# Kernel tuning notes

Hardware: AMD Instinct MI355X
Metric: run time of the kernel (lower is better)

The kernel has to match this reference:

```python
import jax, jax.numpy as jnp
import numpy as np

B, S, D, H = 4, 2048, 1024, 16
DK = D // H  # 64


def setup_inputs() -> dict:
    key = jax.random.key(0)
    ks = jax.random.split(key, 7)
    scale = 1.0 / np.sqrt(D)
    q = jax.random.normal(ks[0], (B, S, D), dtype=jnp.float32)
    k = jax.random.normal(ks[1], (B, S, D), dtype=jnp.float32)
    v = jax.random.normal(ks[2], (B, S, D), dtype=jnp.float32)
    # causal mask, broadcastable to [B, H, S, S]
    mask = jnp.tril(jnp.ones((S, S), dtype=jnp.int32))[None, None, :, :]
    Wq = jax.random.normal(ks[3], (D, D), dtype=jnp.float32) * scale
    Wk = jax.random.normal(ks[4], (D, D), dtype=jnp.float32) * scale
    Wv = jax.random.normal(ks[5], (D, D), dtype=jnp.float32) * scale
    Wo = jax.random.normal(ks[6], (D, D), dtype=jnp.float32) * scale
    return {"q": q, "k": k, "v": v, "mask": mask,
            "Wq": Wq, "Wk": Wk, "Wv": Wv, "Wo": Wo}


def reference(q, k, v, mask, Wq, Wk, Wv, Wo):
    # nn.Linear(bias=False): y = x @ W.T
    query = jnp.einsum('bsd,ed->bse', q, Wq).reshape(B, S, H, DK).transpose(0, 2, 1, 3)
    key_ = jnp.einsum('bsd,ed->bse', k, Wk).reshape(B, S, H, DK).transpose(0, 2, 1, 3)
    value = jnp.einsum('bsd,ed->bse', v, Wv).reshape(B, S, H, DK).transpose(0, 2, 1, 3)
    scores = jnp.einsum('bhqd,bhkd->bhqk', query, key_) / jnp.sqrt(jnp.float32(DK))
    scores = jnp.where(mask == 0, -jnp.inf, scores)
    probs = jax.nn.softmax(scores, axis=-1)
    x = jnp.einsum('bhqk,bhkd->bhqd', probs, value)  # [B,H,S,DK]
    x = x.transpose(0, 2, 1, 3).reshape(B, S, D)
    return jnp.einsum('bsd,ed->bse', x, Wo)
```

## Files before the change

### kernel.cpp

```cpp
#include <hip/hip_runtime.h>
#include <hip/hip_bf16.h>

constexpr int Bn = 4, Sn = 2048, Dn = 1024, Hn = 16, DKn = 64;
constexpr int Mrows = Bn * Sn;
constexpr int NQB = Sn / 64;

typedef __attribute__((ext_vector_type(8))) short short8;
typedef __attribute__((ext_vector_type(4))) float f32x4;
typedef __attribute__((ext_vector_type(4))) unsigned int u32x4;

#define DEV __device__ __forceinline__

constexpr float QSCL = 0.18033688f;

DEV unsigned short f2bf(float f) {
    unsigned u = __builtin_bit_cast(unsigned, f);
    u += 0x7FFFu + ((u >> 16) & 1u);
    return (unsigned short)(u >> 16);
}
DEV unsigned pk2(float a, float b) {
    __hip_bfloat162 h = __float22bfloat162_rn(float2{a, b});
    unsigned u;
    __builtin_memcpy(&u, &h, 4);
    return u;
}
DEV float exp2a(float x) {
    float r;
    asm("v_exp_f32 %0, %1" : "=v"(r) : "v"(x));
    return r;
}

__global__ __launch_bounds__(256) void cvt_w(const float* __restrict__ W0,
                                             const float* __restrict__ W1,
                                             const float* __restrict__ W2,
                                             const float* __restrict__ W3,
                                             unsigned short* __restrict__ Out) {
    const float* src = blockIdx.y == 0 ? W0
                     : blockIdx.y == 1 ? W1
                     : blockIdx.y == 2 ? W2 : W3;
    size_t off = ((size_t)blockIdx.x * 256 + threadIdx.x) * 8;
    const float4* s = (const float4*)(src + off);
    float4 a = s[0], b = s[1];
    u32x4 p = {pk2(a.x, a.y), pk2(a.z, a.w), pk2(b.x, b.y), pk2(b.z, b.w)};
    *(u32x4*)(Out + (size_t)blockIdx.y * (Dn * Dn) + off) = p;
}

template <bool ABF16, bool BBF16, bool OUTF32>
DEV void gemm_body(const void* __restrict__ Ap, const void* __restrict__ Bw,
                   void* __restrict__ Out, float oscale, int m0, int n0) {
    __shared__ alignas(16) unsigned short As[128 * 72];
    __shared__ alignas(16) unsigned short Bs[128 * 72];

    const int tid = threadIdx.x;
    const int lane = tid & 63;
    const int w = tid >> 6;
    const int wm = (w >> 1) * 32;
    const int wn = (w & 1) * 64;
    const int g = lane >> 4, q15 = lane & 15;

    f32x4 acc[2][4] = {};

    const int srow = tid >> 2, sseg = tid & 3;

    const float* Af = (const float*)Ap;
    const unsigned short* Ab = (const unsigned short*)Ap;
    const float* Bf = (const float*)Bw;
    const unsigned short* Bb = (const unsigned short*)Bw;

    float4 fa[4], fb[4];
    u32x4 ua[2], ub[2];

    auto loadA = [&](int kk) {
        if constexpr (ABF16) {
            const u32x4* s =
                (const u32x4*)(Ab + (size_t)(m0 + srow) * Dn + kk + sseg * 16);
            ua[0] = s[0];
            ua[1] = s[1];
        } else {
            const float4* s =
                (const float4*)(Af + (size_t)(m0 + srow) * Dn + kk + sseg * 16);
            fa[0] = s[0]; fa[1] = s[1]; fa[2] = s[2]; fa[3] = s[3];
        }
    };
    auto loadB = [&](int kk) {
        if constexpr (BBF16) {
            const u32x4* s =
                (const u32x4*)(Bb + (size_t)(n0 + srow) * Dn + kk + sseg * 16);
            ub[0] = s[0];
            ub[1] = s[1];
        } else {
            const float4* s =
                (const float4*)(Bf + (size_t)(n0 + srow) * Dn + kk + sseg * 16);
            fb[0] = s[0]; fb[1] = s[1]; fb[2] = s[2]; fb[3] = s[3];
        }
    };
    auto store = [&]() {
        u32x4* da = (u32x4*)(&As[srow * 72 + sseg * 16]);
        if constexpr (ABF16) {
            da[0] = ua[0];
            da[1] = ua[1];
        } else {
            u32x4 p0 = {pk2(fa[0].x, fa[0].y), pk2(fa[0].z, fa[0].w),
                        pk2(fa[1].x, fa[1].y), pk2(fa[1].z, fa[1].w)};
            u32x4 p1 = {pk2(fa[2].x, fa[2].y), pk2(fa[2].z, fa[2].w),
                        pk2(fa[3].x, fa[3].y), pk2(fa[3].z, fa[3].w)};
            da[0] = p0;
            da[1] = p1;
        }
        u32x4* db = (u32x4*)(&Bs[srow * 72 + sseg * 16]);
        if constexpr (BBF16) {
            db[0] = ub[0];
            db[1] = ub[1];
        } else {
            u32x4 q0 = {pk2(fb[0].x, fb[0].y), pk2(fb[0].z, fb[0].w),
                        pk2(fb[1].x, fb[1].y), pk2(fb[1].z, fb[1].w)};
            u32x4 q1 = {pk2(fb[2].x, fb[2].y), pk2(fb[2].z, fb[2].w),
                        pk2(fb[3].x, fb[3].y), pk2(fb[3].z, fb[3].w)};
            db[0] = q0;
            db[1] = q1;
        }
    };

    loadA(0);
    loadB(0);
    for (int kk = 0; kk < Dn; kk += 64) {
        store();
        __syncthreads();
        if (kk + 64 < Dn) {
            loadA(kk + 64);
            loadB(kk + 64);
        }

#pragma unroll
        for (int ks = 0; ks < 2; ++ks) {
            short8 af[2], bf4[4];
#pragma unroll
            for (int mf = 0; mf < 2; ++mf)
                af[mf] = __builtin_bit_cast(
                    short8, *(const u32x4*)(&As[(wm + mf * 16 + q15) * 72 +
                                                ks * 32 + g * 8]));
#pragma unroll
            for (int nf = 0; nf < 4; ++nf)
                bf4[nf] = __builtin_bit_cast(
                    short8, *(const u32x4*)(&Bs[(wn + nf * 16 + q15) * 72 +
                                                ks * 32 + g * 8]));
#pragma unroll
            for (int mf = 0; mf < 2; ++mf)
#pragma unroll
                for (int nf = 0; nf < 4; ++nf)
                    acc[mf][nf] = __builtin_amdgcn_mfma_f32_16x16x32_bf16(
                        af[mf], bf4[nf], acc[mf][nf], 0, 0, 0);
        }
        __syncthreads();
    }

#pragma unroll
    for (int mf = 0; mf < 2; ++mf)
#pragma unroll
        for (int nf = 0; nf < 4; ++nf)
#pragma unroll
            for (int r = 0; r < 4; ++r) {
                int m = m0 + wm + mf * 16 + 4 * g + r;
                int n = n0 + wn + nf * 16 + q15;
                float val = acc[mf][nf][r] * oscale;
                if (OUTF32) {
                    ((float*)Out)[(size_t)m * Dn + n] = val;
                } else {
                    int b = m >> 11, s = m & (Sn - 1);
                    int h = n >> 6, dk = n & 63;
                    ((unsigned short*)Out)[(((size_t)(b * Hn + h) * Sn + s) << 6) +
                                           dk] = f2bf(val);
                }
            }
}

template <bool ABF16, bool BBF16, bool OUTF32>
__global__ __launch_bounds__(512) void gemm_nt(const void* __restrict__ Ap,
                                               const void* __restrict__ Bw,
                                               void* __restrict__ Out,
                                               float oscale) {
    const int bid = (int)(blockIdx.y * gridDim.x + blockIdx.x);
    const int xcd = bid & 7;
    const int jj = bid >> 3;
    const int m0 = (xcd + ((jj & 7) << 3)) * 128;
    const int n0 = (jj >> 3) * 128;
    gemm_body<ABF16, BBF16, OUTF32>(Ap, Bw, Out, oscale, m0, n0);
}

__global__ __launch_bounds__(512) void gemm_qkv(
    const float* __restrict__ q, const float* __restrict__ k,
    const float* __restrict__ v, const unsigned short* __restrict__ Wb,
    unsigned short* __restrict__ Qb, unsigned short* __restrict__ Kb,
    unsigned short* __restrict__ Vb) {
    const int bid = (int)blockIdx.x;
    const int xcd = bid & 7;
    const int jj = bid >> 3;
    const int z = jj >> 6;
    const int inner = jj & 63;
    const int m0 = (xcd + ((inner & 7) << 3)) * 128;
    const int n0 = (inner >> 3) * 128;
    const float* A = z == 0 ? q : z == 1 ? k : v;
    const unsigned short* W = Wb + (size_t)z * Dn * Dn;
    unsigned short* Out = z == 0 ? Qb : z == 1 ? Kb : Vb;
    const float osc = z == 0 ? QSCL : 1.0f;
    gemm_body<false, true, false>(A, W, Out, osc, m0, n0);
}

__global__ __launch_bounds__(512) void attn_fwd(
    const unsigned short* __restrict__ Qb, const unsigned short* __restrict__ Kb,
    const unsigned short* __restrict__ Vb, unsigned short* __restrict__ Xb) {
    __shared__ alignas(16) unsigned short Kt[64 * 64];
    __shared__ alignas(16) unsigned short Vt[64 * 64];

    const int tid = threadIdx.x;
    const int bid = (int)blockIdx.x;
    const int pair = (bid >> 3) & 7;
    const int bh = ((bid >> 6) << 3) + (bid & 7);
    const int b = bh >> 4, h = bh & 15;
    const int lane = tid & 63, w = tid >> 6;
    const int g = lane >> 4, q15 = lane & 15;

    const unsigned short* Qh = Qb + (size_t)bh * Sn * DKn;
    const unsigned short* Kh = Kb + (size_t)bh * Sn * DKn;
    const unsigned short* Vh = Vb + (size_t)bh * Sn * DKn;

    const int st_row = tid >> 3, st_seg = tid & 7;
    const int sv_kv = tid & 63, sv_g = tid >> 6;
    const int sel = sv_kv & 1;
    const int kv_even = sv_kv & ~1;
    const unsigned kvp = (unsigned)(((kv_even & 32) | ((kv_even & 12) << 1) |
                                     ((kv_even & 16) >> 2) | (kv_even & 3)) *
                                    2);

    const short8 ones = {0x3F80, 0x3F80, 0x3F80, 0x3F80,
                         0x3F80, 0x3F80, 0x3F80, 0x3F80};

    u32x4 kr0, vr0;
    auto load_kv = [&](int j) {
        kr0 = *(const u32x4*)(Kh + (size_t)(j * 64 + st_row) * DKn + st_seg * 8);
        vr0 = *(const u32x4*)(Vh + (size_t)(j * 64 + sv_kv) * DKn + sv_g * 8);
    };

    for (int hp = 0; hp < 2; ++hp) {
        const int c = hp == 0 ? (15 - pair) : pair;
        const int jmax = 2 * c + 1;
        const int jdiag = 2 * c + (w >> 2);
        const int qg = c * 128 + w * 16 + q15;

        short8 qf[2];
#pragma unroll
        for (int ks = 0; ks < 2; ++ks)
            qf[ks] = __builtin_bit_cast(
                short8, *(const u32x4*)(Qh + (size_t)qg * DKn + ks * 32 + g * 8));

        f32x4 xacc[4] = {};
        f32x4 xl = {};
        float m_run = -1e30f;

        load_kv(0);
        for (int j = 0; j <= jmax; ++j) {
            {
                unsigned b0 = ((unsigned)(st_row * 128 + st_seg * 16)) ^
                              ((unsigned)(st_row & 7) << 4);
                *(u32x4*)((char*)Kt + b0) = kr0;
            }
            {
                int dk0 = sv_g * 8;
#pragma unroll
                for (int i = 0; i < 4; ++i) {
                    unsigned mine = vr0[i];
                    unsigned theirs = (unsigned)__shfl_xor((int)mine, 1);
                    int dk_abs = dk0 + 2 * i + sel;
                    unsigned out = sel ? ((theirs >> 16) | (mine & 0xffff0000u))
                                       : ((mine & 0xffffu) | (theirs << 16));
                    unsigned byteoff = ((unsigned)(dk_abs * 128) + kvp) ^
                                       ((unsigned)(dk_abs & 7) << 4);
                    *(unsigned*)((char*)Vt + byteoff) = out;
                }
            }
            __syncthreads();

            if (j < jmax) load_kv(j + 1);

            if (j <= jdiag) {
                f32x4 sacc[4] = {};
#pragma unroll
                for (int mf = 0; mf < 4; ++mf) {
                    int row = mf * 16 + q15;
#pragma unroll
                    for (int ks = 0; ks < 2; ++ks) {
                        unsigned byteoff =
                            ((unsigned)(row * 128 + ks * 64 + g * 16)) ^
                            ((unsigned)(row & 7) << 4);
                        short8 kf = __builtin_bit_cast(
                            short8, *(const u32x4*)((char*)Kt + byteoff));
                        sacc[mf] = __builtin_amdgcn_mfma_f32_16x16x32_bf16(
                            kf, qf[ks], sacc[mf], 0, 0, 0);
                    }
                }

                float p[4][4];
                float pmax = -1e30f;
                const bool diag = (j == jdiag);
#pragma unroll
                for (int mf = 0; mf < 4; ++mf)
#pragma unroll
                    for (int r = 0; r < 4; ++r) {
                        float sv = sacc[mf][r];
                        if (diag) {
                            int kvg = j * 64 + mf * 16 + 4 * g + r;
                            if (kvg > qg) sv = -1e30f;
                        }
                        p[mf][r] = sv;
                        pmax = fmaxf(pmax, sv);
                    }
                pmax = fmaxf(pmax, __shfl_xor(pmax, 16));
                pmax = fmaxf(pmax, __shfl_xor(pmax, 32));
                if (__any(pmax > m_run + 8.f)) {
                    float mnew = fmaxf(m_run, pmax);
                    float corr = exp2a(m_run - mnew);
#pragma unroll
                    for (int mf = 0; mf < 4; ++mf)
#pragma unroll
                        for (int r = 0; r < 4; ++r) xacc[mf][r] *= corr;
#pragma unroll
                    for (int r = 0; r < 4; ++r) xl[r] *= corr;
                    m_run = mnew;
                }
#pragma unroll
                for (int mf = 0; mf < 4; ++mf)
#pragma unroll
                    for (int r = 0; r < 4; ++r)
                        p[mf][r] = exp2a(p[mf][r] - m_run);

                unsigned pkk[4][2];
#pragma unroll
                for (int mf = 0; mf < 4; ++mf) {
                    pkk[mf][0] = pk2(p[mf][0], p[mf][1]);
                    pkk[mf][1] = pk2(p[mf][2], p[mf][3]);
                }
#pragma unroll
                for (int ks = 0; ks < 2; ++ks) {
                    u32x4 tmp = {pkk[2 * ks][0], pkk[2 * ks][1],
                                 pkk[2 * ks + 1][0], pkk[2 * ks + 1][1]};
                    short8 pb = __builtin_bit_cast(short8, tmp);
                    xl = __builtin_amdgcn_mfma_f32_16x16x32_bf16(ones, pb, xl,
                                                                 0, 0, 0);
#pragma unroll
                    for (int mf = 0; mf < 4; ++mf) {
                        int row = mf * 16 + q15;
                        unsigned byteoff =
                            ((unsigned)(row * 128 + ks * 64 + g * 16)) ^
                            ((unsigned)(row & 7) << 4);
                        short8 vf = __builtin_bit_cast(
                            short8, *(const u32x4*)((char*)Vt + byteoff));
                        xacc[mf] = __builtin_amdgcn_mfma_f32_16x16x32_bf16(
                            vf, pb, xacc[mf], 0, 0, 0);
                    }
                }
            }
            __syncthreads();
        }

        float inv = 1.0f / xl[0];
        size_t rowbase = (size_t)(b * Sn + c * 128 + w * 16 + q15) * Dn + h * 64;
#pragma unroll
        for (int mf = 0; mf < 4; ++mf) {
            unsigned w0 = pk2(xacc[mf][0] * inv, xacc[mf][1] * inv);
            unsigned w1 = pk2(xacc[mf][2] * inv, xacc[mf][3] * inv);
            uint2 val = {w0, w1};
            *(uint2*)(Xb + rowbase + mf * 16 + 4 * g) = val;
        }
    }
}

extern "C" void kernel_launch(void* const* d_in, const int* in_sizes, int n_in,
                              void* d_out, int out_size, void* d_ws, size_t ws_size,
                              hipStream_t stream) {
    (void)in_sizes; (void)n_in; (void)out_size;
    const float* q = (const float*)d_in[0];
    const float* k = (const float*)d_in[1];
    const float* v = (const float*)d_in[2];
    const float* Wq = (const float*)d_in[4];
    const float* Wk = (const float*)d_in[5];
    const float* Wv = (const float*)d_in[6];
    const float* Wo = (const float*)d_in[7];

    unsigned short* Qb = (unsigned short*)d_ws;
    unsigned short* Kb = Qb + (size_t)Mrows * Dn;
    unsigned short* Vb = Kb + (size_t)Mrows * Dn;
    unsigned short* Xb = Vb + (size_t)Mrows * Dn;
    unsigned short* Wb = Xb + (size_t)Mrows * Dn;

    const size_t needW =
        (size_t)4 * Mrows * Dn * 2 + (size_t)4 * Dn * Dn * 2;
    const bool useWb = ws_size >= needW;

    dim3 blk(256);
    dim3 gblk(512);
    dim3 ggrid(Dn / 128, Mrows / 128);
    dim3 agrid(512);

    if (useWb) {
        cvt_w<<<dim3(Dn * Dn / (256 * 8), 4), blk, 0, stream>>>(Wq, Wk, Wv, Wo, Wb);
        const unsigned short* Wob = Wb + (size_t)3 * Dn * Dn;
        gemm_qkv<<<dim3(1536), gblk, 0, stream>>>(q, k, v, Wb, Qb, Kb, Vb);
        attn_fwd<<<agrid, gblk, 0, stream>>>(Qb, Kb, Vb, Xb);
        gemm_nt<true, true, true><<<ggrid, gblk, 0, stream>>>(Xb, Wob, d_out, 1.0f);
    } else {
        gemm_nt<false, false, false><<<ggrid, gblk, 0, stream>>>(q, Wq, Qb, QSCL);
        gemm_nt<false, false, false><<<ggrid, gblk, 0, stream>>>(k, Wk, Kb, 1.0f);
        gemm_nt<false, false, false><<<ggrid, gblk, 0, stream>>>(v, Wv, Vb, 1.0f);
        attn_fwd<<<agrid, gblk, 0, stream>>>(Qb, Kb, Vb, Xb);
        gemm_nt<true, false, true><<<ggrid, gblk, 0, stream>>>(Xb, Wo, d_out, 1.0f);
    }
}
```

Measured before the change: 183.6 us.

## Process 128-key KV tiles per iteration in attention with per-wave causal skipping

```diff
diff --git a/kernel.cpp b/kernel.cpp
--- a/kernel.cpp
+++ b/kernel.cpp
@@ -3,7 +3,6 @@
 
 constexpr int Bn = 4, Sn = 2048, Dn = 1024, Hn = 16, DKn = 64;
 constexpr int Mrows = Bn * Sn;
-constexpr int NQB = Sn / 64;
 
 typedef __attribute__((ext_vector_type(8))) short short8;
 typedef __attribute__((ext_vector_type(4))) float f32x4;
@@ -209,8 +208,8 @@
 __global__ __launch_bounds__(512) void attn_fwd(
     const unsigned short* __restrict__ Qb, const unsigned short* __restrict__ Kb,
     const unsigned short* __restrict__ Vb, unsigned short* __restrict__ Xb) {
-    __shared__ alignas(16) unsigned short Kt[64 * 64];
-    __shared__ alignas(16) unsigned short Vt[64 * 64];
+    __shared__ alignas(16) unsigned short Kt[2][64 * 64];
+    __shared__ alignas(16) unsigned short Vt[2][64 * 64];
 
     const int tid = threadIdx.x;
     const int bid = (int)blockIdx.x;
@@ -224,10 +223,13 @@
     const unsigned short* Kh = Kb + (size_t)bh * Sn * DKn;
     const unsigned short* Vh = Vb + (size_t)bh * Sn * DKn;
 
-    const int st_row = tid >> 3, st_seg = tid & 7;
-    const int sv_kv = tid & 63, sv_g = tid >> 6;
-    const int sel = sv_kv & 1;
-    const int kv_even = sv_kv & ~1;
+    const int st_row = tid >> 2, st_seg = tid & 3;
+    const int st_half = st_row >> 6, st_rowl = st_row & 63;
+    const int sv_kv = tid & 127, sv_g = tid >> 7;
+    const int sv_half = sv_kv >> 6;
+    const int kvl = sv_kv & 63;
+    const int sel = kvl & 1;
+    const int kv_even = kvl & ~1;
     const unsigned kvp = (unsigned)(((kv_even & 32) | ((kv_even & 12) << 1) |
                                      ((kv_even & 16) >> 2) | (kv_even & 3)) *
                                     2);
@@ -235,16 +237,17 @@
     const short8 ones = {0x3F80, 0x3F80, 0x3F80, 0x3F80,
                          0x3F80, 0x3F80, 0x3F80, 0x3F80};
 
-    u32x4 kr0, vr0;
+    u32x4 kr0, kr1, vr0, vr1;
     auto load_kv = [&](int j) {
-        kr0 = *(const u32x4*)(Kh + (size_t)(j * 64 + st_row) * DKn + st_seg * 8);
-        vr0 = *(const u32x4*)(Vh + (size_t)(j * 64 + sv_kv) * DKn + sv_g * 8);
+        kr0 = *(const u32x4*)(Kh + (size_t)(j * 128 + st_row) * DKn + st_seg * 8);
+        kr1 = *(const u32x4*)(Kh + (size_t)(j * 128 + st_row) * DKn +
+                              (st_seg + 4) * 8);
+        vr0 = *(const u32x4*)(Vh + (size_t)(j * 128 + sv_kv) * DKn + sv_g * 8);
+        vr1 = *(const u32x4*)(Vh + (size_t)(j * 128 + sv_kv) * DKn + sv_g * 8 + 32);
     };
 
     for (int hp = 0; hp < 2; ++hp) {
         const int c = hp == 0 ? (15 - pair) : pair;
-        const int jmax = 2 * c + 1;
-        const int jdiag = 2 * c + (w >> 2);
         const int qg = c * 128 + w * 16 + q15;
 
         short8 qf[2];
@@ -258,105 +261,113 @@
         float m_run = -1e30f;
 
         load_kv(0);
-        for (int j = 0; j <= jmax; ++j) {
+        for (int j = 0; j <= c; ++j) {
             {
-                unsigned b0 = ((unsigned)(st_row * 128 + st_seg * 16)) ^
-                              ((unsigned)(st_row & 7) << 4);
-                *(u32x4*)((char*)Kt + b0) = kr0;
+                char* kb = (char*)&Kt[st_half][0];
+                unsigned b0 = ((unsigned)(st_rowl * 128 + st_seg * 16)) ^
+                              ((unsigned)(st_rowl & 7) << 4);
+                unsigned b1 = ((unsigned)(st_rowl * 128 + (st_seg + 4) * 16)) ^
+                              ((unsigned)(st_rowl & 7) << 4);
+                *(u32x4*)(kb + b0) = kr0;
+                *(u32x4*)(kb + b1) = kr1;
             }
             {
-                int dk0 = sv_g * 8;
-#pragma unroll
-                for (int i = 0; i < 4; ++i) {
-                    unsigned mine = vr0[i];
-                    unsigned theirs = (unsigned)__shfl_xor((int)mine, 1);
-                    int dk_abs = dk0 + 2 * i + sel;
-                    unsigned out = sel ? ((theirs >> 16) | (mine & 0xffff0000u))
-                                       : ((mine & 0xffffu) | (theirs << 16));
-                    unsigned byteoff = ((unsigned)(dk_abs * 128) + kvp) ^
-                                       ((unsigned)(dk_abs & 7) << 4);
-                    *(unsigned*)((char*)Vt + byteoff) = out;
+                char* vb = (char*)&Vt[sv_half][0];
+#pragma unroll
+                for (int r2 = 0; r2 < 2; ++r2) {
+                    u32x4 vvec = r2 ? vr1 : vr0;
+                    int dk0 = sv_g * 8 + r2 * 32;
+#pragma unroll
+                    for (int i = 0; i < 4; ++i) {
+                        unsigned mine = vvec[i];
+                        unsigned theirs = (unsigned)__shfl_xor((int)mine, 1);
+                        int dk_abs = dk0 + 2 * i + sel;
+                        unsigned out = sel ? ((theirs >> 16) | (mine & 0xffff0000u))
+                                           : ((mine & 0xffffu) | (theirs << 16));
+                        unsigned byteoff = ((unsigned)(dk_abs * 128) + kvp) ^
+                                           ((unsigned)(dk_abs & 7) << 4);
+                        *(unsigned*)(vb + byteoff) = out;
+                    }
                 }
             }
             __syncthreads();
 
-            if (j < jmax) load_kv(j + 1);
-
-            if (j <= jdiag) {
-                f32x4 sacc[4] = {};
+            if (j < c) load_kv(j + 1);
+
+            const bool diagt = (j == c);
+
+            f32x4 sacc[8] = {};
+#pragma unroll
+            for (int rg = 0; rg < 8; ++rg) {
+                if (diagt && rg > w) continue;
+                const char* kb = (const char*)&Kt[rg >> 2][0];
+                int rowl = (rg & 3) * 16 + q15;
+#pragma unroll
+                for (int ks = 0; ks < 2; ++ks) {
+                    unsigned byteoff = ((unsigned)(rowl * 128 + ks * 64 + g * 16)) ^
+                                       ((unsigned)(rowl & 7) << 4);
+                    short8 kf =
+                        __builtin_bit_cast(short8, *(const u32x4*)(kb + byteoff));
+                    sacc[rg] = __builtin_amdgcn_mfma_f32_16x16x32_bf16(
+                        kf, qf[ks], sacc[rg], 0, 0, 0);
+                }
+            }
+
+            float pmax = -1e30f;
+#pragma unroll
+            for (int rg = 0; rg < 8; ++rg) {
+                if (diagt && rg > w) continue;
+#pragma unroll
+                for (int r = 0; r < 4; ++r) {
+                    float sv = sacc[rg][r];
+                    if (diagt && rg == w) {
+                        if (4 * g + r > q15) sv = -1e30f;
+                        sacc[rg][r] = sv;
+                    }
+                    pmax = fmaxf(pmax, sv);
+                }
+            }
+            pmax = fmaxf(pmax, __shfl_xor(pmax, 16));
+            pmax = fmaxf(pmax, __shfl_xor(pmax, 32));
+            if (__any(pmax > m_run + 8.f)) {
+                float mnew = fmaxf(m_run, pmax);
+                float corr = exp2a(m_run - mnew);
+#pragma unroll
+                for (int mf = 0; mf < 4; ++mf)
+#pragma unroll
+                    for (int r = 0; r < 4; ++r) xacc[mf][r] *= corr;
+#pragma unroll
+                for (int r = 0; r < 4; ++r) xl[r] *= corr;
+                m_run = mnew;
+            }
+            unsigned pkk[8][2] = {};
+#pragma unroll
+            for (int rg = 0; rg < 8; ++rg) {
+                if (diagt && rg > w) continue;
+#pragma unroll
+                for (int r = 0; r < 4; ++r)
+                    sacc[rg][r] = exp2a(sacc[rg][r] - m_run);
+                pkk[rg][0] = pk2(sacc[rg][0], sacc[rg][1]);
+                pkk[rg][1] = pk2(sacc[rg][2], sacc[rg][3]);
+            }
+
+#pragma unroll
+            for (int ks = 0; ks < 4; ++ks) {
+                u32x4 tmp = {pkk[2 * ks][0], pkk[2 * ks][1], pkk[2 * ks + 1][0],
+                             pkk[2 * ks + 1][1]};
+                short8 pb = __builtin_bit_cast(short8, tmp);
+                xl = __builtin_amdgcn_mfma_f32_16x16x32_bf16(ones, pb, xl, 0, 0, 0);
+                const char* vb = (const char*)&Vt[ks >> 1][0];
 #pragma unroll
                 for (int mf = 0; mf < 4; ++mf) {
                     int row = mf * 16 + q15;
-#pragma unroll
-                    for (int ks = 0; ks < 2; ++ks) {
-                        unsigned byteoff =
-                            ((unsigned)(row * 128 + ks * 64 + g * 16)) ^
-                            ((unsigned)(row & 7) << 4);
-                        short8 kf = __builtin_bit_cast(
-                            short8, *(const u32x4*)((char*)Kt + byteoff));
-                        sacc[mf] = __builtin_amdgcn_mfma_f32_16x16x32_bf16(
-                            kf, qf[ks], sacc[mf], 0, 0, 0);
-                    }
-                }
-
-                float p[4][4];
-                float pmax = -1e30f;
-                const bool diag = (j == jdiag);
-#pragma unroll
-                for (int mf = 0; mf < 4; ++mf)
-#pragma unroll
-                    for (int r = 0; r < 4; ++r) {
-                        float sv = sacc[mf][r];
-                        if (diag) {
-                            int kvg = j * 64 + mf * 16 + 4 * g + r;
-                            if (kvg > qg) sv = -1e30f;
-                        }
-                        p[mf][r] = sv;
-                        pmax = fmaxf(pmax, sv);
-                    }
-                pmax = fmaxf(pmax, __shfl_xor(pmax, 16));
-                pmax = fmaxf(pmax, __shfl_xor(pmax, 32));
-                if (__any(pmax > m_run + 8.f)) {
-                    float mnew = fmaxf(m_run, pmax);
-                    float corr = exp2a(m_run - mnew);
-#pragma unroll
-                    for (int mf = 0; mf < 4; ++mf)
-#pragma unroll
-                        for (int r = 0; r < 4; ++r) xacc[mf][r] *= corr;
-#pragma unroll
-                    for (int r = 0; r < 4; ++r) xl[r] *= corr;
-                    m_run = mnew;
-                }
-#pragma unroll
-                for (int mf = 0; mf < 4; ++mf)
-#pragma unroll
-                    for (int r = 0; r < 4; ++r)
-                        p[mf][r] = exp2a(p[mf][r] - m_run);
-
-                unsigned pkk[4][2];
-#pragma unroll
-                for (int mf = 0; mf < 4; ++mf) {
-                    pkk[mf][0] = pk2(p[mf][0], p[mf][1]);
-                    pkk[mf][1] = pk2(p[mf][2], p[mf][3]);
-                }
-#pragma unroll
-                for (int ks = 0; ks < 2; ++ks) {
-                    u32x4 tmp = {pkk[2 * ks][0], pkk[2 * ks][1],
-                                 pkk[2 * ks + 1][0], pkk[2 * ks + 1][1]};
-                    short8 pb = __builtin_bit_cast(short8, tmp);
-                    xl = __builtin_amdgcn_mfma_f32_16x16x32_bf16(ones, pb, xl,
-                                                                 0, 0, 0);
-#pragma unroll
-                    for (int mf = 0; mf < 4; ++mf) {
-                        int row = mf * 16 + q15;
-                        unsigned byteoff =
-                            ((unsigned)(row * 128 + ks * 64 + g * 16)) ^
-                            ((unsigned)(row & 7) << 4);
-                        short8 vf = __builtin_bit_cast(
-                            short8, *(const u32x4*)((char*)Vt + byteoff));
-                        xacc[mf] = __builtin_amdgcn_mfma_f32_16x16x32_bf16(
-                            vf, pb, xacc[mf], 0, 0, 0);
-                    }
+                    unsigned byteoff =
+                        ((unsigned)(row * 128 + (ks & 1) * 64 + g * 16)) ^
+                        ((unsigned)(row & 7) << 4);
+                    short8 vf =
+                        __builtin_bit_cast(short8, *(const u32x4*)(vb + byteoff));
+                    xacc[mf] = __builtin_amdgcn_mfma_f32_16x16x32_bf16(
+                        vf, pb, xacc[mf], 0, 0, 0);
                 }
             }
             __syncthreads();
```

Result: slower. 190.6 us (+3.8%).
